# Optimization experiments

Measured on AMD Instinct MI355X. Metric: run time of the kernel, lower is better.

The kernel has to match this reference:

```python
import jax, jax.numpy as jnp
import numpy as np

N_VARS = 100
MAX_LAG = 10
HIDDEN = 64
E = N_VARS * MAX_LAG  # number of tiny expert MLPs
BATCH = 4096


def setup_inputs() -> dict:
    key = jax.random.key(0)
    k_x, k_w1, k_b1, k_w2, k_b2 = jax.random.split(key, 5)
    x = jax.random.normal(k_x, (BATCH, E), dtype=jnp.float32)
    # PyTorch Linear(1, H): weight [H,1] -> stacked as [E, H]; bias [E, H]
    lim1 = 1.0  # kaiming-uniform-ish bound for fan_in=1
    W1 = jax.random.uniform(k_w1, (E, HIDDEN), dtype=jnp.float32, minval=-lim1, maxval=lim1)
    b1 = jax.random.uniform(k_b1, (E, HIDDEN), dtype=jnp.float32, minval=-lim1, maxval=lim1)
    # Linear(H, n_vars): weight [n_vars,H] -> stacked as [E, H, n_vars]; bias [E, n_vars]
    lim2 = 1.0 / np.sqrt(HIDDEN)
    W2 = jax.random.uniform(k_w2, (E, HIDDEN, N_VARS), dtype=jnp.float32, minval=-lim2, maxval=lim2)
    b2 = jax.random.uniform(k_b2, (E, N_VARS), dtype=jnp.float32, minval=-lim2, maxval=lim2)
    return {"x": x, "W1": W1, "b1": b1, "W2": W2, "b2": b2}


def reference(x, W1, b1, W2, b2):
    # Fused form of: sum_i Linear2_i(relu(Linear1_i(x[:, i:i+1])))
    # h[b,e,h] = relu(x[b,e] * W1[e,h] + b1[e,h])
    h = jax.nn.relu(x[:, :, None] * W1[None, :, :] + b1[None, :, :])  # [B,E,H]
    # sum over experts folded into the contraction: out[b,v] = sum_e h[b,e,:] @ W2[e,:,v]
    out = jnp.einsum("beh,ehv->bv", h, W2) + jnp.sum(b2, axis=0)  # [B,n_vars]
    return out
```

## Files before the change

### kernel.cpp

```cpp
#include <hip/hip_runtime.h>
#include <hip/hip_bf16.h>

#define NV 100
#define HID 64
#define NE 1000
#define NB 4096
#define ESPLIT 32
#define BLOB 4096

typedef __attribute__((ext_vector_type(8))) short short8;
typedef __attribute__((ext_vector_type(4))) float f32x4;

__device__ __align__(16) float g_bsum[NV];

__device__ __forceinline__ short cvtbf(float f) {
    return __builtin_bit_cast(short, (__bf16)f);
}
__device__ __forceinline__ unsigned short f2bf(float f) {
    return (unsigned short)__builtin_bit_cast(short, (__bf16)f);
}
__device__ __forceinline__ float bf2f(unsigned short s) {
    union { unsigned u; float f; } v; v.u = ((unsigned)s) << 16;
    return v.f;
}
__device__ __forceinline__ unsigned pkbf(float a, float b) {
    return (unsigned)f2bf(a) | ((unsigned)f2bf(b) << 16);
}

__device__ __host__ __forceinline__ void esplit_range(int ks, int* pe0, int* pne) {
    int e0 = (ks < 26) ? 32 * ks : 832 + 28 * (ks - 26);
    int ne = (ks < 26) ? 32 : 28;
    *pe0 = e0; *pne = ne;
}

__global__ void bias_kernel(const float* __restrict__ b2) {
    int v = blockIdx.x;
    float s = 0.f;
    for (int e = threadIdx.x; e < NE; e += 256)
        s += b2[e * NV + v];
    __shared__ float red[4];
    for (int off = 32; off; off >>= 1) s += __shfl_down(s, off, 64);
    if ((threadIdx.x & 63) == 0) red[threadIdx.x >> 6] = s;
    __syncthreads();
    if (threadIdx.x == 0) g_bsum[v] = red[0] + red[1] + red[2] + red[3];
}

__global__ void init_kernel(float* __restrict__ out) {
    int idx = blockIdx.x * 256 + threadIdx.x;
    if (idx < NB * NV) out[idx] = g_bsum[idx % NV];
}

__global__ void prepass4(const float* __restrict__ W2, const float* __restrict__ W1,
                         const float* __restrict__ b1, unsigned* __restrict__ blob) {
    __shared__ float t[HID][NV + 1];
    int e = blockIdx.x;
    const float* src = W2 + (size_t)e * (HID * NV);
    for (int i = threadIdx.x; i < HID * NV; i += 256) {
        int hh = i / NV;
        int v = i - hh * NV;
        t[hh][v] = src[i];
    }
    __syncthreads();
    unsigned* dst = blob + (size_t)e * BLOB;
    for (int o = threadIdx.x; o < 3584; o += 256) {
        int f = o >> 8;
        int r = o & 255;
        int l = r >> 2;
        int q = r & 3;
        int ksh = f / 7, tt = f - 7 * ksh;
        int kg = l >> 4, lrow = l & 15;
        int h0 = ksh * 32 + kg * 8 + 2 * q;
        int v = tt * 16 + lrow;
        unsigned val = 0;
        if (v < NV) val = pkbf(t[h0][v], t[h0 + 1][v]);
        dst[o] = val;
    }
    if (threadIdx.x < 64) {
        dst[3584 + threadIdx.x] = __builtin_bit_cast(unsigned, W1[(size_t)e * HID + threadIdx.x]);
        dst[3648 + threadIdx.x] = __builtin_bit_cast(unsigned, b1[(size_t)e * HID + threadIdx.x]);
    }
}

__global__ __launch_bounds__(256, 2) void moe7(
    const float* __restrict__ x, const unsigned* __restrict__ blob,
    float* __restrict__ part)
{
    __shared__ __align__(16) unsigned char smem[65536];
    unsigned short* xts = (unsigned short*)(smem + 49152);

    const int bid = blockIdx.x;
    const int xcd = bid & 7;
    const int jj  = bid >> 3;
    const int ks  = xcd * 4 + (jj & 3);
    const int mb  = jj >> 2;

    const int tid  = threadIdx.x;
    const int lane = tid & 63;
    const int wave = tid >> 6;
    const int lrow = lane & 15;
    const int kg   = lane >> 4;

    const int row0 = mb * 256;
    int e0, ne; esplit_range(ks, &e0, &ne);

    auto stage = [&](int buf, int e) {
        const unsigned* g = blob + (size_t)e * BLOB;
        unsigned* lbase = (unsigned*)(smem + buf * 16384);
        #pragma unroll
        for (int k = 0; k < 4; ++k) {
            int off = (k * 256 + tid) * 4;
            __builtin_amdgcn_global_load_lds(
                (const __attribute__((address_space(1))) unsigned*)(g + off),
                (__attribute__((address_space(3))) unsigned*)(lbase + off),
                16, 0, 0);
        }
    };

    stage(0, e0);
    stage(1, e0 + 1);
    {
        const float* xp = x + (size_t)(row0 + tid) * NE + e0;
        #pragma unroll
        for (int c4 = 0; c4 < 8; ++c4) {
            int eb = c4 * 4;
            if (eb < ne) {
                float4 v = *(const float4*)(xp + eb);
                xts[(eb + 0) * 256 + tid] = f2bf(v.x);
                xts[(eb + 1) * 256 + tid] = f2bf(v.y);
                xts[(eb + 2) * 256 + tid] = f2bf(v.z);
                xts[(eb + 3) * 256 + tid] = f2bf(v.w);
            }
        }
    }
    __syncthreads();

    f32x4 acc[4][7];
    #pragma unroll
    for (int rf = 0; rf < 4; ++rf)
        #pragma unroll
        for (int t = 0; t < 7; ++t)
            acc[rf][t] = (f32x4){0.f, 0.f, 0.f, 0.f};

    int bi = 0;
    for (int ei = 0; ei < ne; ++ei) {
        asm volatile("s_waitcnt vmcnt(4)" ::: "memory");
        __builtin_amdgcn_s_barrier();
        __builtin_amdgcn_sched_barrier(0);

        if (ei + 2 < ne) {
            int b2 = bi + 2; if (b2 >= 3) b2 -= 3;
            stage(b2, e0 + ei + 2);
        }

        const unsigned char* buf = smem + bi * 16384;
        const float* w1p = (const float*)(buf + 14336);
        const float* b1p = (const float*)(buf + 14592);

        float xv[4];
        #pragma unroll
        for (int rf = 0; rf < 4; ++rf)
            xv[rf] = bf2f(xts[ei * 256 + wave * 64 + rf * 16 + lrow]);

        #pragma unroll
        for (int ksh = 0; ksh < 2; ++ksh) {
            const int hb = ksh * 32 + kg * 8;
            float4 wa = *(const float4*)(w1p + hb);
            float4 wb = *(const float4*)(w1p + hb + 4);
            float4 ba = *(const float4*)(b1p + hb);
            float4 bb = *(const float4*)(b1p + hb + 4);

            short8 afr[4];
            #pragma unroll
            for (int rf = 0; rf < 4; ++rf) {
                float xr = xv[rf];
                short8 a;
                a[0] = cvtbf(fmaxf(fmaf(xr, wa.x, ba.x), 0.f));
                a[1] = cvtbf(fmaxf(fmaf(xr, wa.y, ba.y), 0.f));
                a[2] = cvtbf(fmaxf(fmaf(xr, wa.z, ba.z), 0.f));
                a[3] = cvtbf(fmaxf(fmaf(xr, wa.w, ba.w), 0.f));
                a[4] = cvtbf(fmaxf(fmaf(xr, wb.x, bb.x), 0.f));
                a[5] = cvtbf(fmaxf(fmaf(xr, wb.y, bb.y), 0.f));
                a[6] = cvtbf(fmaxf(fmaf(xr, wb.z, bb.z), 0.f));
                a[7] = cvtbf(fmaxf(fmaf(xr, wb.w, bb.w), 0.f));
                afr[rf] = a;
            }

            __builtin_amdgcn_s_setprio(1);
            #pragma unroll
            for (int t = 0; t < 7; ++t) {
                short8 bf = *(const short8*)(buf + ((ksh * 7 + t) << 10) + lane * 16);
                #pragma unroll
                for (int rf = 0; rf < 4; ++rf)
                    acc[rf][t] = __builtin_amdgcn_mfma_f32_16x16x32_bf16(afr[rf], bf, acc[rf][t], 0, 0, 0);
            }
            __builtin_amdgcn_s_setprio(0);
        }
        __builtin_amdgcn_sched_barrier(0);
        bi = (bi + 1 == 3) ? 0 : bi + 1;
    }

    float* dst = part + (size_t)ks * (NB * NV);
    #pragma unroll
    for (int rf = 0; rf < 4; ++rf) {
        #pragma unroll
        for (int t = 0; t < 7; ++t) {
            int col = t * 16 + lrow;
            if (col < NV) {
                size_t base = (size_t)(row0 + wave * 64 + rf * 16 + kg * 4) * NV + col;
                #pragma unroll
                for (int r = 0; r < 4; ++r)
                    dst[base + (size_t)r * NV] = acc[rf][t][r];
            }
        }
    }
}

__global__ void reduce2(const float* __restrict__ part, float* __restrict__ out) {
    int i4 = blockIdx.x * 256 + threadIdx.x;
    f32x4 s = *(const f32x4*)&g_bsum[(i4 % 25) * 4];
    size_t off = (size_t)i4 * 4;
    #pragma unroll 4
    for (int k = 0; k < ESPLIT; ++k)
        s += *(const f32x4*)&part[(size_t)k * (NB * NV) + off];
    *(f32x4*)&out[off] = s;
}

#define LDW 72
__global__ __launch_bounds__(256, 3) void moe_fallback(
    const float* __restrict__ x, const float* __restrict__ W1,
    const float* __restrict__ b1, const float* __restrict__ W2,
    float* __restrict__ dst)
{
    __shared__ unsigned short w2t[8192];
    const int tid  = threadIdx.x;
    const int lane = tid & 63;
    const int lrow = lane & 15;
    const int kg   = lane >> 4;
    const int wave = tid >> 6;
    const int row0 = blockIdx.x * 128 + wave * 32;
    const int e0 = blockIdx.y * 32;
    const int e1 = min(NE, e0 + 32);

    f32x4 acc[2][7];
    #pragma unroll
    for (int rf = 0; rf < 2; ++rf)
        #pragma unroll
        for (int t = 0; t < 7; ++t)
            acc[rf][t] = (f32x4){0.f, 0.f, 0.f, 0.f};

    const float* xr0 = x + (size_t)(row0 + lrow) * NE;
    const float* xr1 = x + (size_t)(row0 + 16 + lrow) * NE;

    for (int e = e0; e < e1; ++e) {
        __syncthreads();
        const float* src = W2 + (size_t)e * (HID * NV);
        unsigned* w2t32 = (unsigned*)w2t;
        #pragma unroll
        for (int k = 0; k < 13; ++k) {
            int i = tid + k * 256;
            if (i < (HID / 2) * NV) {
                int a3  = i / 400;
                int rem = i - a3 * 400;
                int bv  = rem >> 2;
                int c   = rem & 3;
                int hh2 = a3 * 4 + c;
                float f0 = src[(2 * hh2) * NV + bv];
                float f1 = src[(2 * hh2 + 1) * NV + bv];
                w2t32[bv * (LDW / 2) + hh2] = pkbf(f0, f1);
            }
        }
        __syncthreads();

        float xv0 = xr0[e];
        float xv1 = xr1[e];
        const float* w1p = W1 + e * HID;
        const float* b1p = b1 + e * HID;
        #pragma unroll
        for (int ksh = 0; ksh < 2; ++ksh) {
            const int hb = ksh * 32 + kg * 8;
            f32x4 w1lo = *(const f32x4*)(w1p + hb);
            f32x4 w1hi = *(const f32x4*)(w1p + hb + 4);
            f32x4 blo  = *(const f32x4*)(b1p + hb);
            f32x4 bhi  = *(const f32x4*)(b1p + hb + 4);
            short8 a0, a1;
            #pragma unroll
            for (int j = 0; j < 4; ++j) {
                a0[j]     = cvtbf(fmaxf(fmaf(xv0, w1lo[j], blo[j]), 0.f));
                a0[j + 4] = cvtbf(fmaxf(fmaf(xv0, w1hi[j], bhi[j]), 0.f));
                a1[j]     = cvtbf(fmaxf(fmaf(xv1, w1lo[j], blo[j]), 0.f));
                a1[j + 4] = cvtbf(fmaxf(fmaf(xv1, w1hi[j], bhi[j]), 0.f));
            }
            #pragma unroll
            for (int t = 0; t < 7; ++t) {
                short8 bf = *(const short8*)&w2t[(t * 16 + lrow) * LDW + hb];
                acc[0][t] = __builtin_amdgcn_mfma_f32_16x16x32_bf16(a0, bf, acc[0][t], 0, 0, 0);
                acc[1][t] = __builtin_amdgcn_mfma_f32_16x16x32_bf16(a1, bf, acc[1][t], 0, 0, 0);
            }
        }
    }

    #pragma unroll
    for (int rf = 0; rf < 2; ++rf) {
        #pragma unroll
        for (int t = 0; t < 7; ++t) {
            int col = t * 16 + lrow;
            if (col < NV) {
                size_t base = (size_t)(row0 + rf * 16 + kg * 4) * NV + col;
                #pragma unroll
                for (int r = 0; r < 4; ++r)
                    atomicAdd(&dst[base + (size_t)r * NV], acc[rf][t][r]);
            }
        }
    }
}

extern "C" void kernel_launch(void* const* d_in, const int* in_sizes, int n_in,
                              void* d_out, int out_size, void* d_ws, size_t ws_size,
                              hipStream_t stream) {
    const float* x  = (const float*)d_in[0];
    const float* W1 = (const float*)d_in[1];
    const float* b1 = (const float*)d_in[2];
    const float* W2 = (const float*)d_in[3];
    const float* b2 = (const float*)d_in[4];
    float* out = (float*)d_out;

    const size_t BLOB_BYTES = (size_t)NE * BLOB * 4;
    const size_t PART_BYTES = (size_t)ESPLIT * NB * NV * 4;

    bias_kernel<<<NV, 256, 0, stream>>>(b2);

    if (ws_size >= BLOB_BYTES + PART_BYTES) {
        unsigned* blob = (unsigned*)d_ws;
        float* part = (float*)((char*)d_ws + BLOB_BYTES);
        prepass4<<<NE, 256, 0, stream>>>(W2, W1, b1, blob);
        moe7<<<512, 256, 0, stream>>>(x, blob, part);
        reduce2<<<(NB * NV / 4 + 255) / 256, 256, 0, stream>>>(part, out);
    } else {
        init_kernel<<<(NB * NV + 255) / 256, 256, 0, stream>>>(out);
        moe_fallback<<<dim3(NB / 128, ESPLIT), 256, 0, stream>>>(x, W1, b1, W2, out);
    }
}
```

Baseline: 86.74 us.

## Split expert MLP output columns across 8 waves and double-buffer packed blobs

The main kernel moves from 256-thread blocks, where each wave owns 64 rows and all 7 column tiles, to 512-thread blocks, where two wave groups split the column tiles 4 and 3. This halves accumulator registers per wave and raises the occupancy target. W1 and b1 are packed as bf16 pairs, shrinking the per-expert blob and its LDS footprint. The x tile is laid out so each lane reads its four row values with one vector load. The triple-buffered async staging with a vmcnt wait is replaced by double buffering with a full __syncthreads each expert, which may expose more load latency. W1 and b1 also lose precision by being rounded to bf16.

```diff
diff --git a/kernel.cpp b/kernel.cpp
--- a/kernel.cpp
+++ b/kernel.cpp
@@ -6,10 +6,13 @@
 #define NE 1000
 #define NB 4096
 #define ESPLIT 32
-#define BLOB 4096
+#define BLOBU 3648
+#define BUFB 14592
 
 typedef __attribute__((ext_vector_type(8))) short short8;
 typedef __attribute__((ext_vector_type(4))) float f32x4;
+typedef __attribute__((ext_vector_type(4))) unsigned u32x4;
+typedef __attribute__((ext_vector_type(4))) unsigned short u16x4;
 
 __device__ __align__(16) float g_bsum[NV];
 
@@ -22,6 +25,12 @@
 __device__ __forceinline__ float bf2f(unsigned short s) {
     union { unsigned u; float f; } v; v.u = ((unsigned)s) << 16;
     return v.f;
+}
+__device__ __forceinline__ float bcast_lo(unsigned u) {
+    union { unsigned u; float f; } v; v.u = u << 16; return v.f;
+}
+__device__ __forceinline__ float bcast_hi(unsigned u) {
+    union { unsigned u; float f; } v; v.u = u & 0xffff0000u; return v.f;
 }
 __device__ __forceinline__ unsigned pkbf(float a, float b) {
     return (unsigned)f2bf(a) | ((unsigned)f2bf(b) << 16);
@@ -50,7 +59,7 @@
     if (idx < NB * NV) out[idx] = g_bsum[idx % NV];
 }
 
-__global__ void prepass4(const float* __restrict__ W2, const float* __restrict__ W1,
+__global__ void prepass5(const float* __restrict__ W2, const float* __restrict__ W1,
                          const float* __restrict__ b1, unsigned* __restrict__ blob) {
     __shared__ float t[HID][NV + 1];
     int e = blockIdx.x;
@@ -61,7 +70,7 @@
         t[hh][v] = src[i];
     }
     __syncthreads();
-    unsigned* dst = blob + (size_t)e * BLOB;
+    unsigned* dst = blob + (size_t)e * BLOBU;
     for (int o = threadIdx.x; o < 3584; o += 256) {
         int f = o >> 8;
         int r = o & 255;
@@ -76,17 +85,17 @@
         dst[o] = val;
     }
     if (threadIdx.x < 64) {
-        dst[3584 + threadIdx.x] = __builtin_bit_cast(unsigned, W1[(size_t)e * HID + threadIdx.x]);
-        dst[3648 + threadIdx.x] = __builtin_bit_cast(unsigned, b1[(size_t)e * HID + threadIdx.x]);
-    }
-}
-
-__global__ __launch_bounds__(256, 2) void moe7(
+        int j = threadIdx.x;
+        dst[3584 + j] = pkbf(W1[(size_t)e * HID + j], b1[(size_t)e * HID + j]);
+    }
+}
+
+__global__ __launch_bounds__(512, 4) void moe8(
     const float* __restrict__ x, const unsigned* __restrict__ blob,
     float* __restrict__ part)
 {
-    __shared__ __align__(16) unsigned char smem[65536];
-    unsigned short* xts = (unsigned short*)(smem + 49152);
+    __shared__ __align__(16) unsigned char smem[BUFB * 2 + 16384];
+    unsigned short* xts = (unsigned short*)(smem + 2 * BUFB);
 
     const int bid = blockIdx.x;
     const int xcd = bid & 7;
@@ -99,117 +108,132 @@
     const int wave = tid >> 6;
     const int lrow = lane & 15;
     const int kg   = lane >> 4;
+    const int wm   = wave & 3;
+    const int wn   = wave >> 2;
 
     const int row0 = mb * 256;
     int e0, ne; esplit_range(ks, &e0, &ne);
 
-    auto stage = [&](int buf, int e) {
-        const unsigned* g = blob + (size_t)e * BLOB;
-        unsigned* lbase = (unsigned*)(smem + buf * 16384);
-        #pragma unroll
-        for (int k = 0; k < 4; ++k) {
-            int off = (k * 256 + tid) * 4;
-            __builtin_amdgcn_global_load_lds(
-                (const __attribute__((address_space(1))) unsigned*)(g + off),
-                (__attribute__((address_space(3))) unsigned*)(lbase + off),
-                16, 0, 0);
-        }
-    };
-
-    stage(0, e0);
-    stage(1, e0 + 1);
     {
-        const float* xp = x + (size_t)(row0 + tid) * NE + e0;
-        #pragma unroll
-        for (int c4 = 0; c4 < 8; ++c4) {
-            int eb = c4 * 4;
+        int r = tid & 255, half = tid >> 8;
+        int slot = ((r >> 6) & 3) * 64 + (r & 15) * 4 + ((r >> 4) & 3);
+        const float* xp = x + (size_t)(row0 + r) * NE + e0;
+        #pragma unroll
+        for (int c4 = 0; c4 < 4; ++c4) {
+            int eb = half * 16 + c4 * 4;
             if (eb < ne) {
                 float4 v = *(const float4*)(xp + eb);
-                xts[(eb + 0) * 256 + tid] = f2bf(v.x);
-                xts[(eb + 1) * 256 + tid] = f2bf(v.y);
-                xts[(eb + 2) * 256 + tid] = f2bf(v.z);
-                xts[(eb + 3) * 256 + tid] = f2bf(v.w);
-            }
-        }
-    }
+                xts[(eb + 0) * 256 + slot] = f2bf(v.x);
+                xts[(eb + 1) * 256 + slot] = f2bf(v.y);
+                xts[(eb + 2) * 256 + slot] = f2bf(v.z);
+                xts[(eb + 3) * 256 + slot] = f2bf(v.w);
+            }
+        }
+    }
+
+    auto stage = [&](int buf, int e) {
+        const unsigned* g = blob + (size_t)e * BLOBU;
+        unsigned* lbase = (unsigned*)(smem + buf * BUFB);
+        __builtin_amdgcn_global_load_lds(
+            (const __attribute__((address_space(1))) unsigned*)(g + tid * 4),
+            (__attribute__((address_space(3))) unsigned*)(lbase + tid * 4),
+            16, 0, 0);
+        if (tid < 400)
+            __builtin_amdgcn_global_load_lds(
+                (const __attribute__((address_space(1))) unsigned*)(g + (512 + tid) * 4),
+                (__attribute__((address_space(3))) unsigned*)(lbase + (512 + tid) * 4),
+                16, 0, 0);
+    };
+
+    stage(0, e0);
     __syncthreads();
 
-    f32x4 acc[4][7];
+    f32x4 acc[4][4];
     #pragma unroll
     for (int rf = 0; rf < 4; ++rf)
         #pragma unroll
-        for (int t = 0; t < 7; ++t)
-            acc[rf][t] = (f32x4){0.f, 0.f, 0.f, 0.f};
-
-    int bi = 0;
+        for (int tt = 0; tt < 4; ++tt)
+            acc[rf][tt] = (f32x4){0.f, 0.f, 0.f, 0.f};
+
+    int cur = 0;
     for (int ei = 0; ei < ne; ++ei) {
-        asm volatile("s_waitcnt vmcnt(4)" ::: "memory");
-        __builtin_amdgcn_s_barrier();
-        __builtin_amdgcn_sched_barrier(0);
-
-        if (ei + 2 < ne) {
-            int b2 = bi + 2; if (b2 >= 3) b2 -= 3;
-            stage(b2, e0 + ei + 2);
-        }
-
-        const unsigned char* buf = smem + bi * 16384;
-        const float* w1p = (const float*)(buf + 14336);
-        const float* b1p = (const float*)(buf + 14592);
-
+        if (ei + 1 < ne) stage(cur ^ 1, e0 + ei + 1);
+
+        const unsigned char* bufc = smem + cur * BUFB;
+
+        u16x4 xq = *(const u16x4*)&xts[ei * 256 + wm * 64 + lrow * 4];
         float xv[4];
         #pragma unroll
-        for (int rf = 0; rf < 4; ++rf)
-            xv[rf] = bf2f(xts[ei * 256 + wave * 64 + rf * 16 + lrow]);
+        for (int rf = 0; rf < 4; ++rf) xv[rf] = bf2f(xq[rf]);
 
         #pragma unroll
         for (int ksh = 0; ksh < 2; ++ksh) {
-            const int hb = ksh * 32 + kg * 8;
-            float4 wa = *(const float4*)(w1p + hb);
-            float4 wb = *(const float4*)(w1p + hb + 4);
-            float4 ba = *(const float4*)(b1p + hb);
-            float4 bb = *(const float4*)(b1p + hb + 4);
+            const unsigned char* wpk = bufc + 14336 + ksh * 128 + kg * 32;
+            u32x4 p0 = *(const u32x4*)(wpk);
+            u32x4 p1 = *(const u32x4*)(wpk + 16);
 
             short8 afr[4];
             #pragma unroll
-            for (int rf = 0; rf < 4; ++rf) {
-                float xr = xv[rf];
-                short8 a;
-                a[0] = cvtbf(fmaxf(fmaf(xr, wa.x, ba.x), 0.f));
-                a[1] = cvtbf(fmaxf(fmaf(xr, wa.y, ba.y), 0.f));
-                a[2] = cvtbf(fmaxf(fmaf(xr, wa.z, ba.z), 0.f));
-                a[3] = cvtbf(fmaxf(fmaf(xr, wa.w, ba.w), 0.f));
-                a[4] = cvtbf(fmaxf(fmaf(xr, wb.x, bb.x), 0.f));
-                a[5] = cvtbf(fmaxf(fmaf(xr, wb.y, bb.y), 0.f));
-                a[6] = cvtbf(fmaxf(fmaf(xr, wb.z, bb.z), 0.f));
-                a[7] = cvtbf(fmaxf(fmaf(xr, wb.w, bb.w), 0.f));
-                afr[rf] = a;
+            for (int q = 0; q < 4; ++q) {
+                float w0 = bcast_lo(p0[q]), b0 = bcast_hi(p0[q]);
+                float w1 = bcast_lo(p1[q]), b1v = bcast_hi(p1[q]);
+                #pragma unroll
+                for (int rf = 0; rf < 4; ++rf) {
+                    afr[rf][q]     = cvtbf(fmaxf(fmaf(xv[rf], w0, b0), 0.f));
+                    afr[rf][q + 4] = cvtbf(fmaxf(fmaf(xv[rf], w1, b1v), 0.f));
+                }
             }
 
             __builtin_amdgcn_s_setprio(1);
-            #pragma unroll
-            for (int t = 0; t < 7; ++t) {
-                short8 bf = *(const short8*)(buf + ((ksh * 7 + t) << 10) + lane * 16);
-                #pragma unroll
-                for (int rf = 0; rf < 4; ++rf)
-                    acc[rf][t] = __builtin_amdgcn_mfma_f32_16x16x32_bf16(afr[rf], bf, acc[rf][t], 0, 0, 0);
+            if (wn == 0) {
+                #pragma unroll
+                for (int tt = 0; tt < 4; ++tt) {
+                    short8 bf = *(const short8*)(bufc + ((ksh * 7 + tt) << 10) + lane * 16);
+                    #pragma unroll
+                    for (int rf = 0; rf < 4; ++rf)
+                        acc[rf][tt] = __builtin_amdgcn_mfma_f32_16x16x32_bf16(afr[rf], bf, acc[rf][tt], 0, 0, 0);
+                }
+            } else {
+                #pragma unroll
+                for (int tt = 0; tt < 3; ++tt) {
+                    short8 bf = *(const short8*)(bufc + ((ksh * 7 + 4 + tt) << 10) + lane * 16);
+                    #pragma unroll
+                    for (int rf = 0; rf < 4; ++rf)
+                        acc[rf][tt] = __builtin_amdgcn_mfma_f32_16x16x32_bf16(afr[rf], bf, acc[rf][tt], 0, 0, 0);
+                }
             }
             __builtin_amdgcn_s_setprio(0);
         }
-        __builtin_amdgcn_sched_barrier(0);
-        bi = (bi + 1 == 3) ? 0 : bi + 1;
+        __syncthreads();
+        cur ^= 1;
     }
 
     float* dst = part + (size_t)ks * (NB * NV);
-    #pragma unroll
-    for (int rf = 0; rf < 4; ++rf) {
-        #pragma unroll
-        for (int t = 0; t < 7; ++t) {
-            int col = t * 16 + lrow;
-            if (col < NV) {
-                size_t base = (size_t)(row0 + wave * 64 + rf * 16 + kg * 4) * NV + col;
+    const int rowb = row0 + wm * 64 + kg * 4;
+    if (wn == 0) {
+        #pragma unroll
+        for (int rf = 0; rf < 4; ++rf) {
+            #pragma unroll
+            for (int tt = 0; tt < 4; ++tt) {
+                int col = tt * 16 + lrow;
+                size_t base = (size_t)(rowb + rf * 16) * NV + col;
                 #pragma unroll
                 for (int r = 0; r < 4; ++r)
-                    dst[base + (size_t)r * NV] = acc[rf][t][r];
+                    dst[base + (size_t)r * NV] = acc[rf][tt][r];
+            }
+        }
+    } else {
+        #pragma unroll
+        for (int rf = 0; rf < 4; ++rf) {
+            #pragma unroll
+            for (int tt = 0; tt < 3; ++tt) {
+                int col = (4 + tt) * 16 + lrow;
+                if (col < NV) {
+                    size_t base = (size_t)(rowb + rf * 16) * NV + col;
+                    #pragma unroll
+                    for (int r = 0; r < 4; ++r)
+                        dst[base + (size_t)r * NV] = acc[rf][tt][r];
+                }
             }
         }
     }
@@ -324,7 +348,7 @@
     const float* b2 = (const float*)d_in[4];
     float* out = (float*)d_out;
 
-    const size_t BLOB_BYTES = (size_t)NE * BLOB * 4;
+    const size_t BLOB_BYTES = (size_t)NE * BLOBU * 4;
     const size_t PART_BYTES = (size_t)ESPLIT * NB * NV * 4;
 
     bias_kernel<<<NV, 256, 0, stream>>>(b2);
@@ -332,8 +356,8 @@
     if (ws_size >= BLOB_BYTES + PART_BYTES) {
         unsigned* blob = (unsigned*)d_ws;
         float* part = (float*)((char*)d_ws + BLOB_BYTES);
-        prepass4<<<NE, 256, 0, stream>>>(W2, W1, b1, blob);
-        moe7<<<512, 256, 0, stream>>>(x, blob, part);
+        prepass5<<<NE, 256, 0, stream>>>(W2, W1, b1, blob);
+        moe8<<<512, 512, 0, stream>>>(x, blob, part);
         reduce2<<<(NB * NV / 4 + 255) / 256, 256, 0, stream>>>(part, out);
     } else {
         init_kernel<<<(NB * NV + 255) / 256, 256, 0, stream>>>(out);
```

Result: slower. 131.7 us (+51.9%).

## Pack blob tighter and double-buffer expert pairs with one barrier per pair

Applied to the files above, without the earlier changes.

Shrinks each expert's packed blob from 4096 to 3712 words by interleaving W1/b1 per lane group. The main kernel now stages two experts at a time into double-buffered LDS and syncs once per pair instead of once per expert with a triple buffer. It also relayouts x in LDS so each lane fetches its four rows with one vector load. The intent is fewer barriers, fewer LDS reads and less blob traffic. The pairing assumes an even expert count per split, and the waits on the async LDS loads are now implicit in __syncthreads. LDS use grows to about 75KB per block, which may limit blocks per CU.

```diff
diff --git a/kernel.cpp b/kernel.cpp
--- a/kernel.cpp
+++ b/kernel.cpp
@@ -6,10 +6,12 @@
 #define NE 1000
 #define NB 4096
 #define ESPLIT 32
-#define BLOB 4096
+#define BLOBU 3712
+#define EXPB 14848
 
 typedef __attribute__((ext_vector_type(8))) short short8;
 typedef __attribute__((ext_vector_type(4))) float f32x4;
+typedef __attribute__((ext_vector_type(4))) unsigned short u16x4;
 
 __device__ __align__(16) float g_bsum[NV];
 
@@ -50,7 +52,7 @@
     if (idx < NB * NV) out[idx] = g_bsum[idx % NV];
 }
 
-__global__ void prepass4(const float* __restrict__ W2, const float* __restrict__ W1,
+__global__ void prepass6(const float* __restrict__ W2, const float* __restrict__ W1,
                          const float* __restrict__ b1, unsigned* __restrict__ blob) {
     __shared__ float t[HID][NV + 1];
     int e = blockIdx.x;
@@ -61,7 +63,7 @@
         t[hh][v] = src[i];
     }
     __syncthreads();
-    unsigned* dst = blob + (size_t)e * BLOB;
+    unsigned* dst = blob + (size_t)e * BLOBU;
     for (int o = threadIdx.x; o < 3584; o += 256) {
         int f = o >> 8;
         int r = o & 255;
@@ -75,18 +77,22 @@
         if (v < NV) val = pkbf(t[h0][v], t[h0 + 1][v]);
         dst[o] = val;
     }
-    if (threadIdx.x < 64) {
-        dst[3584 + threadIdx.x] = __builtin_bit_cast(unsigned, W1[(size_t)e * HID + threadIdx.x]);
-        dst[3648 + threadIdx.x] = __builtin_bit_cast(unsigned, b1[(size_t)e * HID + threadIdx.x]);
-    }
-}
-
-__global__ __launch_bounds__(256, 2) void moe7(
+    if (threadIdx.x < 128) {
+        int o = threadIdx.x;
+        int ksh = o >> 6, kg = (o >> 4) & 3, j = o & 15;
+        int h0 = ksh * 32 + kg * 8;
+        float val = (j < 8) ? W1[(size_t)e * HID + h0 + j]
+                            : b1[(size_t)e * HID + h0 + (j - 8)];
+        dst[3584 + o] = __builtin_bit_cast(unsigned, val);
+    }
+}
+
+__global__ __launch_bounds__(256, 2) void moe9(
     const float* __restrict__ x, const unsigned* __restrict__ blob,
     float* __restrict__ part)
 {
-    __shared__ __align__(16) unsigned char smem[65536];
-    unsigned short* xts = (unsigned short*)(smem + 49152);
+    __shared__ __align__(16) unsigned char smem[4 * EXPB + 16384];
+    unsigned short* xts = (unsigned short*)(smem + 4 * EXPB);
 
     const int bid = blockIdx.x;
     const int xcd = bid & 7;
@@ -103,35 +109,44 @@
     const int row0 = mb * 256;
     int e0, ne; esplit_range(ks, &e0, &ne);
 
-    auto stage = [&](int buf, int e) {
-        const unsigned* g = blob + (size_t)e * BLOB;
-        unsigned* lbase = (unsigned*)(smem + buf * 16384);
-        #pragma unroll
-        for (int k = 0; k < 4; ++k) {
+    {
+        int r = tid;
+        int slot = (r >> 6) * 64 + (r & 15) * 4 + ((r >> 4) & 3);
+        const float* xp = x + (size_t)(row0 + r) * NE + e0;
+        #pragma unroll
+        for (int c4 = 0; c4 < 8; ++c4) {
+            int eb = c4 * 4;
+            if (eb < ne) {
+                float4 v = *(const float4*)(xp + eb);
+                xts[(eb + 0) * 256 + slot] = f2bf(v.x);
+                xts[(eb + 1) * 256 + slot] = f2bf(v.y);
+                xts[(eb + 2) * 256 + slot] = f2bf(v.z);
+                xts[(eb + 3) * 256 + slot] = f2bf(v.w);
+            }
+        }
+    }
+
+    auto stage2 = [&](int buf, int e) {
+        const unsigned* g = blob + (size_t)e * BLOBU;
+        unsigned* lbase = (unsigned*)(smem + buf * (2 * EXPB));
+        #pragma unroll
+        for (int k = 0; k < 7; ++k) {
             int off = (k * 256 + tid) * 4;
             __builtin_amdgcn_global_load_lds(
                 (const __attribute__((address_space(1))) unsigned*)(g + off),
                 (__attribute__((address_space(3))) unsigned*)(lbase + off),
                 16, 0, 0);
         }
+        if (tid < 64) {
+            int off = (1792 + tid) * 4;
+            __builtin_amdgcn_global_load_lds(
+                (const __attribute__((address_space(1))) unsigned*)(g + off),
+                (__attribute__((address_space(3))) unsigned*)(lbase + off),
+                16, 0, 0);
+        }
     };
 
-    stage(0, e0);
-    stage(1, e0 + 1);
-    {
-        const float* xp = x + (size_t)(row0 + tid) * NE + e0;
-        #pragma unroll
-        for (int c4 = 0; c4 < 8; ++c4) {
-            int eb = c4 * 4;
-            if (eb < ne) {
-                float4 v = *(const float4*)(xp + eb);
-                xts[(eb + 0) * 256 + tid] = f2bf(v.x);
-                xts[(eb + 1) * 256 + tid] = f2bf(v.y);
-                xts[(eb + 2) * 256 + tid] = f2bf(v.z);
-                xts[(eb + 3) * 256 + tid] = f2bf(v.w);
-            }
-        }
-    }
+    stage2(0, e0);
     __syncthreads();
 
     f32x4 acc[4][7];
@@ -141,33 +156,19 @@
         for (int t = 0; t < 7; ++t)
             acc[rf][t] = (f32x4){0.f, 0.f, 0.f, 0.f};
 
-    int bi = 0;
-    for (int ei = 0; ei < ne; ++ei) {
-        asm volatile("s_waitcnt vmcnt(4)" ::: "memory");
-        __builtin_amdgcn_s_barrier();
-        __builtin_amdgcn_sched_barrier(0);
-
-        if (ei + 2 < ne) {
-            int b2 = bi + 2; if (b2 >= 3) b2 -= 3;
-            stage(b2, e0 + ei + 2);
-        }
-
-        const unsigned char* buf = smem + bi * 16384;
-        const float* w1p = (const float*)(buf + 14336);
-        const float* b1p = (const float*)(buf + 14592);
-
+    auto do_expert = [&](const unsigned char* ebase, int ei) {
+        u16x4 xq = *(const u16x4*)&xts[ei * 256 + wave * 64 + lrow * 4];
         float xv[4];
         #pragma unroll
-        for (int rf = 0; rf < 4; ++rf)
-            xv[rf] = bf2f(xts[ei * 256 + wave * 64 + rf * 16 + lrow]);
+        for (int rf = 0; rf < 4; ++rf) xv[rf] = bf2f(xq[rf]);
 
         #pragma unroll
         for (int ksh = 0; ksh < 2; ++ksh) {
-            const int hb = ksh * 32 + kg * 8;
-            float4 wa = *(const float4*)(w1p + hb);
-            float4 wb = *(const float4*)(w1p + hb + 4);
-            float4 ba = *(const float4*)(b1p + hb);
-            float4 bb = *(const float4*)(b1p + hb + 4);
+            const float4* wpk = (const float4*)(ebase + 14336 + (ksh * 4 + kg) * 64);
+            float4 wa = wpk[0];
+            float4 wb = wpk[1];
+            float4 ba = wpk[2];
+            float4 bb = wpk[3];
 
             short8 afr[4];
             #pragma unroll
@@ -188,15 +189,26 @@
             __builtin_amdgcn_s_setprio(1);
             #pragma unroll
             for (int t = 0; t < 7; ++t) {
-                short8 bf = *(const short8*)(buf + ((ksh * 7 + t) << 10) + lane * 16);
+                short8 bf = *(const short8*)(ebase + ((ksh * 7 + t) << 10) + lane * 16);
                 #pragma unroll
                 for (int rf = 0; rf < 4; ++rf)
                     acc[rf][t] = __builtin_amdgcn_mfma_f32_16x16x32_bf16(afr[rf], bf, acc[rf][t], 0, 0, 0);
             }
             __builtin_amdgcn_s_setprio(0);
         }
-        __builtin_amdgcn_sched_barrier(0);
-        bi = (bi + 1 == 3) ? 0 : bi + 1;
+    };
+
+    int cur = 0;
+    const int npairs = ne >> 1;
+    for (int p = 0; p < npairs; ++p) {
+        if (p + 1 < npairs) stage2(cur ^ 1, e0 + 2 * (p + 1));
+
+        const unsigned char* bufc = smem + cur * (2 * EXPB);
+        do_expert(bufc, 2 * p);
+        do_expert(bufc + EXPB, 2 * p + 1);
+
+        __syncthreads();
+        cur ^= 1;
     }
 
     float* dst = part + (size_t)ks * (NB * NV);
@@ -324,7 +336,7 @@
     const float* b2 = (const float*)d_in[4];
     float* out = (float*)d_out;
 
-    const size_t BLOB_BYTES = (size_t)NE * BLOB * 4;
+    const size_t BLOB_BYTES = (size_t)NE * BLOBU * 4;
     const size_t PART_BYTES = (size_t)ESPLIT * NB * NV * 4;
 
     bias_kernel<<<NV, 256, 0, stream>>>(b2);
@@ -332,8 +344,8 @@
     if (ws_size >= BLOB_BYTES + PART_BYTES) {
         unsigned* blob = (unsigned*)d_ws;
         float* part = (float*)((char*)d_ws + BLOB_BYTES);
-        prepass4<<<NE, 256, 0, stream>>>(W2, W1, b1, blob);
-        moe7<<<512, 256, 0, stream>>>(x, blob, part);
+        prepass6<<<NE, 256, 0, stream>>>(W2, W1, b1, blob);
+        moe9<<<512, 256, 0, stream>>>(x, blob, part);
         reduce2<<<(NB * NV / 4 + 255) / 256, 256, 0, stream>>>(part, out);
     } else {
         init_kernel<<<(NB * NV + 255) / 256, 256, 0, stream>>>(out);
```

Measured after the change: 81.57 us. 6.0% less time.
